# Kernel optimization log

Measured on AMD Instinct MI355X. Metric: run time of the kernel, lower is better.

## Reference

```python
import jax, jax.numpy as jnp
import numpy as np

N_NODES = 50000
N_EDGES = 1600000
N_GRAPHS = 128
DIM_IN = 128
DIM_SELF = 16


def setup_inputs() -> dict:
    key = jax.random.key(0)
    ks = jax.random.split(key, 12)
    feat = jax.random.normal(ks[0], (N_NODES, DIM_IN), dtype=jnp.float32)
    self_feat = jax.random.normal(ks[1], (N_GRAPHS, DIM_SELF), dtype=jnp.float32)
    src = jax.random.randint(ks[2], (N_EDGES,), 0, N_NODES)
    dst = jax.random.randint(ks[3], (N_EDGES,), 0, N_NODES)
    graph_id = jnp.sort(jax.random.randint(ks[4], (N_NODES,), 0, N_GRAPHS))
    def lin(k, fan_in, fan_out):
        bound = 1.0 / np.sqrt(fan_in)
        return jax.random.uniform(k, (fan_in, fan_out), dtype=jnp.float32, minval=-bound, maxval=bound)
    W1 = lin(ks[5], DIM_IN, 100)
    b1 = jnp.zeros((100,), jnp.float32)
    W2 = lin(ks[6], 100, 20)
    b2 = jnp.zeros((20,), jnp.float32)
    Wf1 = lin(ks[7], 20 + DIM_SELF, 10)
    bf1 = jnp.zeros((10,), jnp.float32)
    Wf2 = lin(ks[8], 10, 1)
    bf2 = jnp.zeros((1,), jnp.float32)
    return {"feat": feat, "self_feat": self_feat, "src": src, "dst": dst,
            "graph_id": graph_id, "W1": W1, "b1": b1, "W2": W2, "b2": b2,
            "Wf1": Wf1, "bf1": bf1, "Wf2": Wf2, "bf2": bf2}


def _gcn_layer(h, src, dst, deg, W, b):
    # copy_u gather over edges + mean segment reduce over dst, then linear apply
    msg_sum = jax.ops.segment_sum(h[src], dst, num_segments=h.shape[0])  # [N, d]
    mean = msg_sum / jnp.maximum(deg, 1.0)[:, None]
    # DGL update_all leaves zero-in-degree nodes with their prior feature
    h_agg = jnp.where((deg > 0)[:, None], mean, h)
    return h_agg @ W + b


def reference(feat, self_feat, src, dst, graph_id, W1, b1, W2, b2, Wf1, bf1, Wf2, bf2):
    n = feat.shape[0]
    deg = jax.ops.segment_sum(jnp.ones((src.shape[0],), feat.dtype), dst, num_segments=n)
    h = jax.nn.relu(_gcn_layer(feat, src, dst, deg, W1, b1))   # [N,100]
    h = jax.nn.relu(_gcn_layer(h, src, dst, deg, W2, b2))      # [N,20]
    # dgl.mean_nodes: per-graph mean of node features
    g_sum = jax.ops.segment_sum(h, graph_id, num_segments=N_GRAPHS)  # [G,20]
    g_cnt = jax.ops.segment_sum(jnp.ones((n,), h.dtype), graph_id, num_segments=N_GRAPHS)
    hg = g_sum / jnp.maximum(g_cnt, 1.0)[:, None]
    fused = jnp.concatenate([hg, self_feat], axis=1)           # [G, 20+dim_self]
    out = jax.nn.relu(fused @ Wf1 + bf1) @ Wf2 + bf2           # [G, dim_out]
    return out
```

## Files before the change

### kernel.cpp

```cpp
#include <hip/hip_runtime.h>

constexpr int NN = 50000;
constexpr int NE = 1600000;
constexpr int NG = 128;
constexpr int BSTRIDE = 96;

constexpr int FILL_PASSES = 8;
constexpr int NODES_PER_PASS = 6250;
constexpr int BLOCKS_PER_PASS = (NE + 255) / 256;

constexpr int A1_NODES = 36;
constexpr int A1_BLOCKS = (NN + A1_NODES - 1) / A1_NODES;

#define OFF_CNT      0
#define OFF_GSUM     200000
#define OFF_GCNT     210240
#define ZERO_BYTES   210752
#define OFF_ADJ      210752
#define OFF_X1F      9810816
#define OFF_X2B      16210816

typedef float v2f __attribute__((ext_vector_type(2)));

__device__ __forceinline__ unsigned short f2bf(float x) {
    unsigned int v = __float_as_uint(x);
    return (unsigned short)((v + 0x7FFFu + ((v >> 16) & 1u)) >> 16);
}
__device__ __forceinline__ float bflo(unsigned int u) { return __uint_as_float(u << 16); }
__device__ __forceinline__ float bfhi(unsigned int u) { return __uint_as_float(u & 0xFFFF0000u); }

__global__ void k_fill(const int* __restrict__ src, const int* __restrict__ dst,
                       int* __restrict__ cnt, unsigned short* __restrict__ adj) {
    const int pass = blockIdx.x & 7;
    const int chunk = blockIdx.x >> 3;
    const int i = chunk * 256 + threadIdx.x;
    if (i >= NE) return;
    const int d = __builtin_nontemporal_load(dst + i);
    const int lo = pass * NODES_PER_PASS;
    if (d >= lo && d < lo + NODES_PER_PASS) {
        const int p = atomicAdd(&cnt[d], 1);
        const int s = __builtin_nontemporal_load(src + i);
        if (p < BSTRIDE) adj[d * BSTRIDE + p] = (unsigned short)s;
    }
}

__global__ __launch_bounds__(256) void k_gemm1(const float4* __restrict__ feat4,
                                               const float* __restrict__ W1,
                                               unsigned int* __restrict__ X1f) {
    const int t = threadIdx.x;
    if (t >= 250) return;
    const int cg = t % 25;
    const int nq = t / 25;
    const int node0 = blockIdx.x * 40 + nq * 4;
    const int col0 = cg * 4;

    float acc[4][4];
#pragma unroll
    for (int i = 0; i < 4; ++i)
#pragma unroll
        for (int j = 0; j < 4; ++j) acc[i][j] = 0.f;

    for (int k4 = 0; k4 < 32; ++k4) {
        float4 f[4];
#pragma unroll
        for (int i = 0; i < 4; ++i) f[i] = feat4[(node0 + i) * 32 + k4];
        float4 wr[4];
#pragma unroll
        for (int kk = 0; kk < 4; ++kk)
            wr[kk] = *(const float4*)(W1 + (k4 * 4 + kk) * 100 + col0);
#pragma unroll
        for (int kk = 0; kk < 4; ++kk) {
#pragma unroll
            for (int i = 0; i < 4; ++i) {
                const float fv = (kk == 0) ? f[i].x
                               : (kk == 1) ? f[i].y
                               : (kk == 2) ? f[i].z : f[i].w;
                acc[i][0] += fv * wr[kk].x;
                acc[i][1] += fv * wr[kk].y;
                acc[i][2] += fv * wr[kk].z;
                acc[i][3] += fv * wr[kk].w;
            }
        }
    }
#pragma unroll
    for (int i = 0; i < 4; ++i) {
        int u = 0;
        u = __builtin_amdgcn_cvt_pk_fp8_f32(acc[i][0], acc[i][1], u, false);
        u = __builtin_amdgcn_cvt_pk_fp8_f32(acc[i][2], acc[i][3], u, true);
        X1f[(node0 + i) * 32 + cg] = (unsigned int)u;
        if (cg == 24) {
#pragma unroll
            for (int z = 25; z < 32; ++z) X1f[(node0 + i) * 32 + z] = 0u;
        }
    }
}

__global__ __launch_bounds__(256) void k_agg1g2(
        const uint4* __restrict__ X1u, const int* __restrict__ cnt,
        const unsigned short* __restrict__ adj, const float* __restrict__ b1,
        const float* __restrict__ W2, unsigned int* __restrict__ X2b) {
    __shared__ float hl[A1_NODES * 100];
    __shared__ float w2s[100 * 20];
    const int t = threadIdx.x;
    const int node0 = blockIdx.x * A1_NODES;
    for (int i = t; i < 2000; i += 256) w2s[i] = W2[i];

    if (t < A1_NODES * 7) {
        const int nl = t / 7;
        const int q = t - nl * 7;
        const int node = node0 + nl;
        if (node < NN) {
            const int d = cnt[node];
            const unsigned short* ab = adj + node * BSTRIDE;
            float a[16];
#pragma unroll
            for (int j = 0; j < 16; ++j) a[j] = 0.f;

#define ACC4(UU, B) { v2f l_ = __builtin_amdgcn_cvt_pk_f32_fp8((int)(UU), false); \
                      v2f h_ = __builtin_amdgcn_cvt_pk_f32_fp8((int)(UU), true);  \
                      a[B+0] += l_.x; a[B+1] += l_.y; a[B+2] += h_.x; a[B+3] += h_.y; }
#define SET4(UU, B) { v2f l_ = __builtin_amdgcn_cvt_pk_f32_fp8((int)(UU), false); \
                      v2f h_ = __builtin_amdgcn_cvt_pk_f32_fp8((int)(UU), true);  \
                      a[B+0] = l_.x; a[B+1] = l_.y; a[B+2] = h_.x; a[B+3] = h_.y; }

            for (int i = 0; i < d; ++i) {
                const int s = (int)ab[i];
                const uint4 u = X1u[s * 8 + q];
                ACC4(u.x, 0) ACC4(u.y, 4) ACC4(u.z, 8) ACC4(u.w, 12)
            }
            if (d > 0) {
                const float inv = 1.f / (float)d;
#pragma unroll
                for (int j = 0; j < 16; ++j) a[j] *= inv;
            } else {
                const uint4 u = X1u[node * 8 + q];
                SET4(u.x, 0) SET4(u.y, 4) SET4(u.z, 8) SET4(u.w, 12)
            }
#undef ACC4
#undef SET4
            const int col0 = 16 * q;
            float* hrow = hl + nl * 100 + col0;
            const int nc = (q < 6) ? 16 : 4;
#pragma unroll 4
            for (int j = 0; j < nc; ++j)
                hrow[j] = fmaxf(a[j] + b1[col0 + j], 0.f);
        }
    }
    __syncthreads();

    for (int idx = t; idx < A1_NODES * 16; idx += 256) {
        const int nl = idx >> 4;
        const int node = node0 + nl;
        if (node >= NN) break;
        const int j = idx & 15;
        unsigned int o = 0u;
        if (j < 10) {
            const float* h = hl + nl * 100;
            float a0 = 0.f, a1 = 0.f;
#pragma unroll 5
            for (int k = 0; k < 100; ++k) {
                const float hv = h[k];
                a0 += hv * w2s[k * 20 + 2 * j];
                a1 += hv * w2s[k * 20 + 2 * j + 1];
            }
            o = (unsigned int)f2bf(a0) | ((unsigned int)f2bf(a1) << 16);
        }
        X2b[node * 16 + j] = o;
    }
}

__global__ __launch_bounds__(320) void k_agg2(const uint2* __restrict__ X2v,
                                              const int* __restrict__ cnt,
                                              const unsigned short* __restrict__ adj,
                                              const float* __restrict__ b2,
                                              const int* __restrict__ graph_id,
                                              float* __restrict__ g_sum,
                                              float* __restrict__ g_cnt) {
    __shared__ float lsum[NG * 20];
    __shared__ float lcnt[NG];
    const int t = threadIdx.x;
    for (int i = t; i < NG * 20; i += 320) lsum[i] = 0.f;
    for (int i = t; i < NG; i += 320) lcnt[i] = 0.f;
    __syncthreads();

    const int node = blockIdx.x * 64 + t / 5;
    const int q = t % 5;
    if (node < NN) {
        const int d = cnt[node];
        const unsigned short* ab = adj + node * BSTRIDE;
        float ax = 0.f, ay = 0.f, az = 0.f, aw = 0.f;
        for (int i = 0; i < d; ++i) {
            const int s = (int)ab[i];
            const uint2 u = X2v[s * 8 + q];
            ax += bflo(u.x); ay += bfhi(u.x);
            az += bflo(u.y); aw += bfhi(u.y);
        }
        if (d > 0) {
            const float inv = 1.f / (float)d;
            ax *= inv; ay *= inv; az *= inv; aw *= inv;
        } else {
            const uint2 u = X2v[node * 8 + q];
            ax = bflo(u.x); ay = bfhi(u.x);
            az = bflo(u.y); aw = bfhi(u.y);
        }
        const int col0 = 4 * q;
        const float hx = fmaxf(ax + b2[col0 + 0], 0.f);
        const float hy = fmaxf(ay + b2[col0 + 1], 0.f);
        const float hz = fmaxf(az + b2[col0 + 2], 0.f);
        const float hw = fmaxf(aw + b2[col0 + 3], 0.f);
        const int g = graph_id[node];
        atomicAdd(&lsum[g * 20 + col0 + 0], hx);
        atomicAdd(&lsum[g * 20 + col0 + 1], hy);
        atomicAdd(&lsum[g * 20 + col0 + 2], hz);
        atomicAdd(&lsum[g * 20 + col0 + 3], hw);
        if (q == 0) atomicAdd(&lcnt[g], 1.f);
    }
    __syncthreads();

    const int first = blockIdx.x * 64;
    const int last = min(first + 63, NN - 1);
    const int gmin = graph_id[first];
    const int span = graph_id[last] - gmin + 1;
    for (int idx = t; idx < span * 20; idx += 320) {
        const int g = gmin + idx / 20;
        const int c = idx - (idx / 20) * 20;
        const float v = lsum[g * 20 + c];
        if (v != 0.f) atomicAdd(&g_sum[g * 20 + c], v);
    }
    for (int idx = t; idx < span; idx += 320) {
        const float v = lcnt[gmin + idx];
        if (v != 0.f) atomicAdd(&g_cnt[gmin + idx], v);
    }
}

__global__ __launch_bounds__(128) void k_final(const float* __restrict__ g_sum,
                                               const float* __restrict__ g_cnt,
                                               const float* __restrict__ self_feat,
                                               const float* __restrict__ Wf1,
                                               const float* __restrict__ bf1,
                                               const float* __restrict__ Wf2,
                                               const float* __restrict__ bf2,
                                               float* __restrict__ out) {
    const int g = threadIdx.x;
    float fused[36];
    const float cnt = fmaxf(g_cnt[g], 1.f);
    const float inv = 1.f / cnt;
#pragma unroll
    for (int j = 0; j < 20; ++j) fused[j] = g_sum[g * 20 + j] * inv;
#pragma unroll
    for (int j = 0; j < 16; ++j) fused[20 + j] = self_feat[g * 16 + j];
    float o = bf2[0];
#pragma unroll
    for (int i = 0; i < 10; ++i) {
        float t = bf1[i];
#pragma unroll
        for (int k = 0; k < 36; ++k) t += fused[k] * Wf1[k * 10 + i];
        o += fmaxf(t, 0.f) * Wf2[i];
    }
    out[g] = o;
}

extern "C" void kernel_launch(void* const* d_in, const int* in_sizes, int n_in,
                              void* d_out, int out_size, void* d_ws, size_t ws_size,
                              hipStream_t stream) {
    const float* feat      = (const float*)d_in[0];
    const float* self_feat = (const float*)d_in[1];
    const int*   src       = (const int*)d_in[2];
    const int*   dst       = (const int*)d_in[3];
    const int*   graph_id  = (const int*)d_in[4];
    const float* W1        = (const float*)d_in[5];
    const float* b1        = (const float*)d_in[6];
    const float* W2        = (const float*)d_in[7];
    const float* b2        = (const float*)d_in[8];
    const float* Wf1       = (const float*)d_in[9];
    const float* bf1       = (const float*)d_in[10];
    const float* Wf2       = (const float*)d_in[11];
    const float* bf2       = (const float*)d_in[12];

    char* w = (char*)d_ws;
    int*            cnt      = (int*)(w + OFF_CNT);
    float*          g_sum    = (float*)(w + OFF_GSUM);
    float*          g_cnt    = (float*)(w + OFF_GCNT);
    unsigned short* adj      = (unsigned short*)(w + OFF_ADJ);
    unsigned int*   X1f      = (unsigned int*)(w + OFF_X1F);
    unsigned int*   X2b      = (unsigned int*)(w + OFF_X2B);

    hipMemsetAsync(w, 0, ZERO_BYTES, stream);

    k_fill<<<FILL_PASSES * BLOCKS_PER_PASS, 256, 0, stream>>>(src, dst, cnt, adj);
    k_gemm1<<<1250, 256, 0, stream>>>((const float4*)feat, W1, X1f);
    k_agg1g2<<<A1_BLOCKS, 256, 0, stream>>>((const uint4*)X1f, cnt, adj, b1,
                                            W2, X2b);
    k_agg2<<<(NN + 63) / 64, 320, 0, stream>>>((const uint2*)X2b, cnt,
                                               adj, b2, graph_id, g_sum, g_cnt);
    k_final<<<1, 128, 0, stream>>>(g_sum, g_cnt, self_feat, Wf1, bf1, Wf2, bf2,
                                   (float*)d_out);
}
```

Before: 297.8 us.

## Bucket edges by destination range before building adjacency lists

Replaces the 8-pass fill kernel, which rescanned every edge once per destination range, with a bucketing pass followed by a fill pass. Each edge is written once as a packed (dst<<16|src) word into one of 8 per-range buckets, using block-local shared-memory counters to reserve space. The fill kernel then does the per-node atomics only over each range's bucket. This cuts the 8x reread of src/dst at the cost of an extra kernel launch and a bucket write and read. The fixed bucket capacity (204800 per range) and 16-bit packing of dst rely on the input distribution and node count, and edges within each range now arrive in a nondeterministic order.

```diff
diff --git a/kernel.cpp b/kernel.cpp
--- a/kernel.cpp
+++ b/kernel.cpp
@@ -5,9 +5,10 @@
 constexpr int NG = 128;
 constexpr int BSTRIDE = 96;
 
-constexpr int FILL_PASSES = 8;
+constexpr int FILL_RANGES = 8;
 constexpr int NODES_PER_PASS = 6250;
-constexpr int BLOCKS_PER_PASS = (NE + 255) / 256;
+constexpr int BUCKET_CAP = 204800;
+constexpr int FILLB_BLOCKS_PER_RANGE = BUCKET_CAP / 256;
 
 constexpr int A1_NODES = 36;
 constexpr int A1_BLOCKS = (NN + A1_NODES - 1) / A1_NODES;
@@ -15,10 +16,12 @@
 #define OFF_CNT      0
 #define OFF_GSUM     200000
 #define OFF_GCNT     210240
-#define ZERO_BYTES   210752
-#define OFF_ADJ      210752
+#define OFF_BCUR     210752
+#define ZERO_BYTES   210784
+#define OFF_ADJ      210816
 #define OFF_X1F      9810816
 #define OFF_X2B      16210816
+#define OFF_BUCKET   19410816
 
 typedef float v2f __attribute__((ext_vector_type(2)));
 
@@ -29,19 +32,42 @@
 __device__ __forceinline__ float bflo(unsigned int u) { return __uint_as_float(u << 16); }
 __device__ __forceinline__ float bfhi(unsigned int u) { return __uint_as_float(u & 0xFFFF0000u); }
 
-__global__ void k_fill(const int* __restrict__ src, const int* __restrict__ dst,
-                       int* __restrict__ cnt, unsigned short* __restrict__ adj) {
-    const int pass = blockIdx.x & 7;
+__global__ __launch_bounds__(256) void k_bucket(const int* __restrict__ src,
+                                                const int* __restrict__ dst,
+                                                int* __restrict__ bcur,
+                                                unsigned int* __restrict__ bucket) {
+    __shared__ int lcnt[FILL_RANGES];
+    __shared__ int lbase[FILL_RANGES];
+    const int t = threadIdx.x;
+    if (t < FILL_RANGES) lcnt[t] = 0;
+    __syncthreads();
+    const int i = blockIdx.x * 256 + t;
+    const int d = dst[i];
+    const int s = src[i];
+    const int r = (unsigned)d / (unsigned)NODES_PER_PASS;
+    const int lp = atomicAdd(&lcnt[r], 1);
+    __syncthreads();
+    if (t < FILL_RANGES) {
+        lbase[t] = (lcnt[t] > 0) ? atomicAdd(&bcur[t], lcnt[t]) : 0;
+    }
+    __syncthreads();
+    bucket[r * BUCKET_CAP + lbase[r] + lp] =
+        ((unsigned int)d << 16) | (unsigned int)s;
+}
+
+__global__ __launch_bounds__(256) void k_fill2(const unsigned int* __restrict__ bucket,
+                                               const int* __restrict__ bcur,
+                                               int* __restrict__ cnt,
+                                               unsigned short* __restrict__ adj) {
+    const int r = blockIdx.x & 7;
     const int chunk = blockIdx.x >> 3;
-    const int i = chunk * 256 + threadIdx.x;
-    if (i >= NE) return;
-    const int d = __builtin_nontemporal_load(dst + i);
-    const int lo = pass * NODES_PER_PASS;
-    if (d >= lo && d < lo + NODES_PER_PASS) {
-        const int p = atomicAdd(&cnt[d], 1);
-        const int s = __builtin_nontemporal_load(src + i);
-        if (p < BSTRIDE) adj[d * BSTRIDE + p] = (unsigned short)s;
-    }
+    const int t = chunk * 256 + threadIdx.x;
+    if (t >= bcur[r]) return;
+    const unsigned int e = bucket[r * BUCKET_CAP + t];
+    const int d = (int)(e >> 16);
+    const int s = (int)(e & 0xFFFFu);
+    const int p = atomicAdd(&cnt[d], 1);
+    if (p < BSTRIDE) adj[d * BSTRIDE + p] = (unsigned short)s;
 }
 
 __global__ __launch_bounds__(256) void k_gemm1(const float4* __restrict__ feat4,
@@ -281,13 +307,17 @@
     int*            cnt      = (int*)(w + OFF_CNT);
     float*          g_sum    = (float*)(w + OFF_GSUM);
     float*          g_cnt    = (float*)(w + OFF_GCNT);
+    int*            bcur     = (int*)(w + OFF_BCUR);
     unsigned short* adj      = (unsigned short*)(w + OFF_ADJ);
     unsigned int*   X1f      = (unsigned int*)(w + OFF_X1F);
     unsigned int*   X2b      = (unsigned int*)(w + OFF_X2B);
+    unsigned int*   bucket   = (unsigned int*)(w + OFF_BUCKET);
 
     hipMemsetAsync(w, 0, ZERO_BYTES, stream);
 
-    k_fill<<<FILL_PASSES * BLOCKS_PER_PASS, 256, 0, stream>>>(src, dst, cnt, adj);
+    k_bucket<<<NE / 256, 256, 0, stream>>>(src, dst, bcur, bucket);
+    k_fill2<<<FILL_RANGES * FILLB_BLOCKS_PER_RANGE, 256, 0, stream>>>(
+        bucket, bcur, cnt, adj);
     k_gemm1<<<1250, 256, 0, stream>>>((const float4*)feat, W1, X1f);
     k_agg1g2<<<A1_BLOCKS, 256, 0, stream>>>((const uint4*)X1f, cnt, adj, b1,
                                             W2, X2b);
```

Measured after the change: 365.1 us. 1.23x slower.

## Split each node's edge list across two half-groups in both aggregation kernels

Applied to the files above, without the earlier changes.

Both aggregation kernels now assign 16 lanes per node, with two halves each summing half of the neighbor list and combining via a cross-lane shuffle. Blocks shrink to 16 nodes, which gives more blocks and more parallel gather streams, shortening the serial per-thread edge loop. The fill kernel also drops its nontemporal loads. In exchange, more lanes sit idle (7 of 8 or 5 of 8 active) and W2 is loaded into shared memory by more blocks. Removing the bounds checks relies on NN being divisible by 16.

```diff
diff --git a/kernel.cpp b/kernel.cpp
--- a/kernel.cpp
+++ b/kernel.cpp
@@ -9,8 +9,9 @@
 constexpr int NODES_PER_PASS = 6250;
 constexpr int BLOCKS_PER_PASS = (NE + 255) / 256;
 
-constexpr int A1_NODES = 36;
-constexpr int A1_BLOCKS = (NN + A1_NODES - 1) / A1_NODES;
+constexpr int A1_NODES = 16;
+constexpr int A1_BLOCKS = NN / A1_NODES;
+constexpr int A2_BLOCKS = NN / 16;
 
 #define OFF_CNT      0
 #define OFF_GSUM     200000
@@ -35,12 +36,11 @@
     const int chunk = blockIdx.x >> 3;
     const int i = chunk * 256 + threadIdx.x;
     if (i >= NE) return;
-    const int d = __builtin_nontemporal_load(dst + i);
+    const int d = dst[i];
     const int lo = pass * NODES_PER_PASS;
     if (d >= lo && d < lo + NODES_PER_PASS) {
         const int p = atomicAdd(&cnt[d], 1);
-        const int s = __builtin_nontemporal_load(src + i);
-        if (p < BSTRIDE) adj[d * BSTRIDE + p] = (unsigned short)s;
+        if (p < BSTRIDE) adj[d * BSTRIDE + p] = (unsigned short)src[i];
     }
 }
 
@@ -105,16 +105,16 @@
     const int node0 = blockIdx.x * A1_NODES;
     for (int i = t; i < 2000; i += 256) w2s[i] = W2[i];
 
-    if (t < A1_NODES * 7) {
-        const int nl = t / 7;
-        const int q = t - nl * 7;
-        const int node = node0 + nl;
-        if (node < NN) {
-            const int d = cnt[node];
-            const unsigned short* ab = adj + node * BSTRIDE;
-            float a[16];
-#pragma unroll
-            for (int j = 0; j < 16; ++j) a[j] = 0.f;
+    const int nl   = t >> 4;
+    const int l    = t & 15;
+    const int q    = l & 7;
+    const int half = l >> 3;
+    const int node = node0 + nl;
+    const int d = cnt[node];
+    const unsigned short* ab = adj + node * BSTRIDE;
+    float a[16];
+#pragma unroll
+    for (int j = 0; j < 16; ++j) a[j] = 0.f;
 
 #define ACC4(UU, B) { v2f l_ = __builtin_amdgcn_cvt_pk_f32_fp8((int)(UU), false); \
                       v2f h_ = __builtin_amdgcn_cvt_pk_f32_fp8((int)(UU), true);  \
@@ -123,53 +123,59 @@
                       v2f h_ = __builtin_amdgcn_cvt_pk_f32_fp8((int)(UU), true);  \
                       a[B+0] = l_.x; a[B+1] = l_.y; a[B+2] = h_.x; a[B+3] = h_.y; }
 
-            for (int i = 0; i < d; ++i) {
+    if (q < 7) {
+        if (d == 0) {
+            if (half == 0) {
+                const uint4 u = X1u[node * 8 + q];
+                SET4(u.x, 0) SET4(u.y, 4) SET4(u.z, 8) SET4(u.w, 12)
+            }
+        } else {
+            const int i0 = half ? (d >> 1) : 0;
+            const int i1 = half ? d : (d >> 1);
+            for (int i = i0; i < i1; ++i) {
                 const int s = (int)ab[i];
                 const uint4 u = X1u[s * 8 + q];
                 ACC4(u.x, 0) ACC4(u.y, 4) ACC4(u.z, 8) ACC4(u.w, 12)
             }
-            if (d > 0) {
-                const float inv = 1.f / (float)d;
-#pragma unroll
-                for (int j = 0; j < 16; ++j) a[j] *= inv;
-            } else {
-                const uint4 u = X1u[node * 8 + q];
-                SET4(u.x, 0) SET4(u.y, 4) SET4(u.z, 8) SET4(u.w, 12)
-            }
+        }
+    }
 #undef ACC4
 #undef SET4
-            const int col0 = 16 * q;
-            float* hrow = hl + nl * 100 + col0;
-            const int nc = (q < 6) ? 16 : 4;
+#pragma unroll
+    for (int j = 0; j < 16; ++j) a[j] += __shfl_xor(a[j], 8);
+
+    if (half == 0 && q < 7) {
+        if (d > 0) {
+            const float inv = 1.f / (float)d;
+#pragma unroll
+            for (int j = 0; j < 16; ++j) a[j] *= inv;
+        }
+        const int col0 = 16 * q;
+        float* hrow = hl + nl * 100 + col0;
+        const int nc = (q < 6) ? 16 : 4;
 #pragma unroll 4
-            for (int j = 0; j < nc; ++j)
-                hrow[j] = fmaxf(a[j] + b1[col0 + j], 0.f);
-        }
+        for (int j = 0; j < nc; ++j)
+            hrow[j] = fmaxf(a[j] + b1[col0 + j], 0.f);
     }
     __syncthreads();
 
-    for (int idx = t; idx < A1_NODES * 16; idx += 256) {
-        const int nl = idx >> 4;
-        const int node = node0 + nl;
-        if (node >= NN) break;
-        const int j = idx & 15;
-        unsigned int o = 0u;
-        if (j < 10) {
-            const float* h = hl + nl * 100;
-            float a0 = 0.f, a1 = 0.f;
+    const int j = t & 15;
+    unsigned int o = 0u;
+    if (j < 10) {
+        const float* h = hl + nl * 100;
+        float a0 = 0.f, a1 = 0.f;
 #pragma unroll 5
-            for (int k = 0; k < 100; ++k) {
-                const float hv = h[k];
-                a0 += hv * w2s[k * 20 + 2 * j];
-                a1 += hv * w2s[k * 20 + 2 * j + 1];
-            }
-            o = (unsigned int)f2bf(a0) | ((unsigned int)f2bf(a1) << 16);
-        }
-        X2b[node * 16 + j] = o;
-    }
-}
-
-__global__ __launch_bounds__(320) void k_agg2(const uint2* __restrict__ X2v,
+        for (int k = 0; k < 100; ++k) {
+            const float hv = h[k];
+            a0 += hv * w2s[k * 20 + 2 * j];
+            a1 += hv * w2s[k * 20 + 2 * j + 1];
+        }
+        o = (unsigned int)f2bf(a0) | ((unsigned int)f2bf(a1) << 16);
+    }
+    X2b[node * 16 + j] = o;
+}
+
+__global__ __launch_bounds__(256) void k_agg2(const uint2* __restrict__ X2v,
                                               const int* __restrict__ cnt,
                                               const unsigned short* __restrict__ adj,
                                               const float* __restrict__ b2,
@@ -179,29 +185,45 @@
     __shared__ float lsum[NG * 20];
     __shared__ float lcnt[NG];
     const int t = threadIdx.x;
-    for (int i = t; i < NG * 20; i += 320) lsum[i] = 0.f;
-    for (int i = t; i < NG; i += 320) lcnt[i] = 0.f;
+    for (int i = t; i < NG * 20; i += 256) lsum[i] = 0.f;
+    if (t < NG) lcnt[t] = 0.f;
     __syncthreads();
 
-    const int node = blockIdx.x * 64 + t / 5;
-    const int q = t % 5;
-    if (node < NN) {
-        const int d = cnt[node];
-        const unsigned short* ab = adj + node * BSTRIDE;
-        float ax = 0.f, ay = 0.f, az = 0.f, aw = 0.f;
-        for (int i = 0; i < d; ++i) {
-            const int s = (int)ab[i];
-            const uint2 u = X2v[s * 8 + q];
-            ax += bflo(u.x); ay += bfhi(u.x);
-            az += bflo(u.y); aw += bfhi(u.y);
-        }
+    const int nl   = t >> 4;
+    const int l    = t & 15;
+    const int q    = l & 7;
+    const int half = l >> 3;
+    const int node = blockIdx.x * 16 + nl;
+    const int d = cnt[node];
+    const unsigned short* ab = adj + node * BSTRIDE;
+    float ax = 0.f, ay = 0.f, az = 0.f, aw = 0.f;
+    if (q < 5) {
+        if (d == 0) {
+            if (half == 0) {
+                const uint2 u = X2v[node * 8 + q];
+                ax = bflo(u.x); ay = bfhi(u.x);
+                az = bflo(u.y); aw = bfhi(u.y);
+            }
+        } else {
+            const int i0 = half ? (d >> 1) : 0;
+            const int i1 = half ? d : (d >> 1);
+            for (int i = i0; i < i1; ++i) {
+                const int s = (int)ab[i];
+                const uint2 u = X2v[s * 8 + q];
+                ax += bflo(u.x); ay += bfhi(u.x);
+                az += bflo(u.y); aw += bfhi(u.y);
+            }
+        }
+    }
+    ax += __shfl_xor(ax, 8);
+    ay += __shfl_xor(ay, 8);
+    az += __shfl_xor(az, 8);
+    aw += __shfl_xor(aw, 8);
+
+    if (half == 0 && q < 5) {
         if (d > 0) {
             const float inv = 1.f / (float)d;
             ax *= inv; ay *= inv; az *= inv; aw *= inv;
-        } else {
-            const uint2 u = X2v[node * 8 + q];
-            ax = bflo(u.x); ay = bfhi(u.x);
-            az = bflo(u.y); aw = bfhi(u.y);
         }
         const int col0 = 4 * q;
         const float hx = fmaxf(ax + b2[col0 + 0], 0.f);
@@ -213,21 +235,20 @@
         atomicAdd(&lsum[g * 20 + col0 + 1], hy);
         atomicAdd(&lsum[g * 20 + col0 + 2], hz);
         atomicAdd(&lsum[g * 20 + col0 + 3], hw);
-        if (q == 0) atomicAdd(&lcnt[g], 1.f);
-    }
+    }
+    if (l == 0) atomicAdd(&lcnt[graph_id[node]], 1.f);
     __syncthreads();
 
-    const int first = blockIdx.x * 64;
-    const int last = min(first + 63, NN - 1);
+    const int first = blockIdx.x * 16;
     const int gmin = graph_id[first];
-    const int span = graph_id[last] - gmin + 1;
-    for (int idx = t; idx < span * 20; idx += 320) {
+    const int span = graph_id[first + 15] - gmin + 1;
+    for (int idx = t; idx < span * 20; idx += 256) {
         const int g = gmin + idx / 20;
         const int c = idx - (idx / 20) * 20;
         const float v = lsum[g * 20 + c];
         if (v != 0.f) atomicAdd(&g_sum[g * 20 + c], v);
     }
-    for (int idx = t; idx < span; idx += 320) {
+    for (int idx = t; idx < span; idx += 256) {
         const float v = lcnt[gmin + idx];
         if (v != 0.f) atomicAdd(&g_cnt[gmin + idx], v);
     }
@@ -291,8 +312,8 @@
     k_gemm1<<<1250, 256, 0, stream>>>((const float4*)feat, W1, X1f);
     k_agg1g2<<<A1_BLOCKS, 256, 0, stream>>>((const uint4*)X1f, cnt, adj, b1,
                                             W2, X2b);
-    k_agg2<<<(NN + 63) / 64, 320, 0, stream>>>((const uint2*)X2b, cnt,
-                                               adj, b2, graph_id, g_sum, g_cnt);
+    k_agg2<<<A2_BLOCKS, 256, 0, stream>>>((const uint2*)X2b, cnt,
+                                          adj, b2, graph_id, g_sum, g_cnt);
     k_final<<<1, 128, 0, stream>>>(g_sum, g_cnt, self_feat, Wf1, bf1, Wf2, bf2,
                                    (float*)d_out);
 }
```

Result: no change. 296.0 us (-0.6%).
